# Kernel tuning notes

Hardware: AMD Instinct MI355X
Metric: run time of the kernel (lower is better)

## Reference

```python
import jax, jax.numpy as jnp
import numpy as np

FP8_MAX = 448.0  # max finite value of float8_e4m3fn


def _fp8_quant_dequant(t, scale):
    """Per-tensor static FP8 e4m3fn quantize -> dequantize (simulated real quant)."""
    q = jnp.clip(t / scale, -FP8_MAX, FP8_MAX).astype(jnp.float8_e4m3fn)
    return q.astype(jnp.float32) * scale


def setup_inputs() -> dict:
    key = jax.random.key(0)
    k1, k2, k3 = jax.random.split(key, 3)
    M, K, N = 4096, 4096, 14336  # tokens, in_features, out_features
    x = jax.random.normal(k1, (M, K), jnp.float32)
    weight = jax.random.normal(k2, (N, K), jnp.float32) * 0.02
    bias = jax.random.normal(k3, (N,), jnp.float32) * 0.01
    # static per-tensor calibration scales (amax / fp8_max)
    input_scale = (jnp.max(jnp.abs(x)) / FP8_MAX).reshape(1)
    weight_scale = (jnp.max(jnp.abs(weight)) / FP8_MAX).reshape(1)
    return {"x": x, "weight": weight, "bias": bias,
            "input_scale": input_scale, "weight_scale": weight_scale}


def reference(x, weight, bias, input_scale, weight_scale):
    # QParamsLinear forward: statically quantize input to fp8 e4m3fn with the
    # input quantizer's per-tensor scale, dequantize the fp8 weight with its
    # per-tensor scale, run the GEMM (y = x_dq @ W_dq^T), and add bias.
    s_in = input_scale[0]
    s_w = weight_scale[0]
    x_dq = _fp8_quant_dequant(x, s_in)      # [M, K]
    w_dq = _fp8_quant_dequant(weight, s_w)  # [N, K]
    return jnp.einsum('mk,nk->mn', x_dq, w_dq) + bias[None, :]
```

## Files before the change

kernel.cpp:

```cpp
#include <hip/hip_runtime.h>
#include <stdint.h>

typedef float f32x4 __attribute__((ext_vector_type(4)));

#define FP8_MAX_V 448.0f

__device__ __forceinline__ uint32_t pack4_fp8(float a, float b, float c, float d) {
    a = fminf(fmaxf(a, -FP8_MAX_V), FP8_MAX_V);
    b = fminf(fmaxf(b, -FP8_MAX_V), FP8_MAX_V);
    c = fminf(fmaxf(c, -FP8_MAX_V), FP8_MAX_V);
    d = fminf(fmaxf(d, -FP8_MAX_V), FP8_MAX_V);
    int v = 0;
    v = __builtin_amdgcn_cvt_pk_fp8_f32(a, b, v, false);
    v = __builtin_amdgcn_cvt_pk_fp8_f32(c, d, v, true);
    return (uint32_t)v;
}

__global__ void quant_fp8_kernel(const float* __restrict__ in,
                                 uint32_t* __restrict__ out,
                                 const float* __restrict__ scale_ptr,
                                 long long n4) {
    const float s = scale_ptr[0];
    long long i = (long long)blockIdx.x * blockDim.x + threadIdx.x;
    const long long stride = (long long)gridDim.x * blockDim.x;
    const float4* in4 = (const float4*)in;
    for (; i < n4; i += stride) {
        float4 v = in4[i];
        out[i] = pack4_fp8(v.x / s, v.y / s, v.z / s, v.w / s);
    }
}

__global__ __launch_bounds__(256) void gemm_fp8_kernel(
    const uint8_t* __restrict__ qA,
    const uint8_t* __restrict__ qB,
    const float* __restrict__ bias,
    const float* __restrict__ s_in_p,
    const float* __restrict__ s_w_p,
    float* __restrict__ C,
    int M, int N, int K) {
    __shared__ uint8_t lsA[128 * 128];
    __shared__ uint8_t lsB[128 * 128];

    const int tid = threadIdx.x;
    const int w   = tid >> 6;
    const int l   = tid & 63;
    const int wr  = w >> 1;
    const int wc  = w & 1;

    const int bm = blockIdx.y << 7;
    const int bn = blockIdx.x << 7;

    const float outscale = s_in_p[0] * s_w_p[0];

    f32x4 acc[4][4];
#pragma unroll
    for (int i = 0; i < 4; ++i)
#pragma unroll
        for (int j = 0; j < 4; ++j)
            acc[i][j] = (f32x4){0.f, 0.f, 0.f, 0.f};

    const int srow = l >> 3;
    const int scol = (((l & 7) ^ srow) << 4);
    const int rsw  = (l & 7) << 4;
    const int lg   = l >> 4;
    const int lr   = l & 15;

    const uint8_t* srcA0 = qA + (size_t)(bm + w * 32 + srow) * K + scol;
    const uint8_t* srcB0 = qB + (size_t)(bn + w * 32 + srow) * K + scol;

    const int nkt = K >> 7;
    for (int kt = 0; kt < nkt; ++kt) {
        const int kb = kt << 7;
#pragma unroll
        for (int i = 0; i < 4; ++i) {
            __builtin_amdgcn_global_load_lds(
                (const __attribute__((address_space(1))) void*)(srcA0 + (size_t)i * 8 * K + kb),
                (__attribute__((address_space(3))) void*)(lsA + (w * 32 + i * 8) * 128),
                16, 0, 0);
        }
#pragma unroll
        for (int i = 0; i < 4; ++i) {
            __builtin_amdgcn_global_load_lds(
                (const __attribute__((address_space(1))) void*)(srcB0 + (size_t)i * 8 * K + kb),
                (__attribute__((address_space(3))) void*)(lsB + (w * 32 + i * 8) * 128),
                16, 0, 0);
        }
        __syncthreads();

#pragma unroll
        for (int kk = 0; kk < 4; ++kk) {
            const int cswz = ((kk << 5) + (lg << 3)) ^ rsw;
            long a[4], b[4];
#pragma unroll
            for (int mi = 0; mi < 4; ++mi)
                a[mi] = *(const long*)(lsA + ((wr * 64 + mi * 16 + lr) << 7) + cswz);
#pragma unroll
            for (int ni = 0; ni < 4; ++ni)
                b[ni] = *(const long*)(lsB + ((wc * 64 + ni * 16 + lr) << 7) + cswz);
#pragma unroll
            for (int mi = 0; mi < 4; ++mi)
#pragma unroll
                for (int ni = 0; ni < 4; ++ni)
                    acc[mi][ni] = __builtin_amdgcn_mfma_f32_16x16x32_fp8_fp8(
                        a[mi], b[ni], acc[mi][ni], 0, 0, 0);
        }
        __syncthreads();
    }

    const int crow0 = bm + wr * 64 + lg * 4;
    const int ccol0 = bn + wc * 64 + lr;
#pragma unroll
    for (int ni = 0; ni < 4; ++ni) {
        const int col = ccol0 + ni * 16;
        const float bv = bias[col];
#pragma unroll
        for (int mi = 0; mi < 4; ++mi) {
            const int row = crow0 + mi * 16;
#pragma unroll
            for (int r = 0; r < 4; ++r)
                C[(size_t)(row + r) * N + col] = acc[mi][ni][r] * outscale + bv;
        }
    }
}

extern "C" void kernel_launch(void* const* d_in, const int* in_sizes, int n_in,
                              void* d_out, int out_size, void* d_ws, size_t ws_size,
                              hipStream_t stream) {
    const float* x    = (const float*)d_in[0];
    const float* wt   = (const float*)d_in[1];
    const float* bias = (const float*)d_in[2];
    const float* s_in = (const float*)d_in[3];
    const float* s_w  = (const float*)d_in[4];
    float* out = (float*)d_out;

    const long long xe = in_sizes[0];
    const long long we = in_sizes[1];
    const int N = in_sizes[2];
    const int K = (int)(we / N);
    const int M = (int)(xe / K);

    uint8_t* qx = (uint8_t*)d_ws;
    uint8_t* qw = qx + xe;

    quant_fp8_kernel<<<2048, 256, 0, stream>>>(x,  (uint32_t*)qx, s_in, xe >> 2);
    quant_fp8_kernel<<<2048, 256, 0, stream>>>(wt, (uint32_t*)qw, s_w,  we >> 2);

    dim3 grid(N / 128, M / 128);
    gemm_fp8_kernel<<<grid, 256, 0, stream>>>(qx, qw, bias, s_in, s_w, out, M, N, K);
}
```

Before: 483.9 us.

## Rewrite FP8 GEMM with 256x128 tiles, 4-stage LDS pipeline and 32x32 MFMA

```diff
diff --git a/kernel.cpp b/kernel.cpp
--- a/kernel.cpp
+++ b/kernel.cpp
@@ -1,7 +1,7 @@
 #include <hip/hip_runtime.h>
 #include <stdint.h>
 
-typedef float f32x4 __attribute__((ext_vector_type(4)));
+typedef float f32x16 __attribute__((ext_vector_type(16)));
 
 #define FP8_MAX_V 448.0f
 
@@ -30,7 +30,7 @@
     }
 }
 
-__global__ __launch_bounds__(256) void gemm_fp8_kernel(
+__global__ __launch_bounds__(512) void gemm_fp8_kernel(
     const uint8_t* __restrict__ qA,
     const uint8_t* __restrict__ qB,
     const float* __restrict__ bias,
@@ -38,89 +38,144 @@
     const float* __restrict__ s_w_p,
     float* __restrict__ C,
     int M, int N, int K) {
-    __shared__ uint8_t lsA[128 * 128];
-    __shared__ uint8_t lsB[128 * 128];
+    extern __shared__ uint8_t lds[];
 
     const int tid = threadIdx.x;
     const int w   = tid >> 6;
     const int l   = tid & 63;
     const int wr  = w >> 1;
     const int wc  = w & 1;
-
-    const int bm = blockIdx.y << 7;
-    const int bn = blockIdx.x << 7;
+    const int rl  = l & 31;
+    const int hi8 = (l >> 5) << 3;
+    const int s2  = (rl >> 1) & 3;
+
+    const int cpx = gridDim.x >> 3;
+    const int swz = ((int)blockIdx.x & 7) * cpx + ((int)blockIdx.x >> 3);
+    const int tm  = swz & 15;
+    const int tn  = swz >> 4;
+    const int bm  = tm << 8;
+    const int bn  = tn << 7;
 
     const float outscale = s_in_p[0] * s_w_p[0];
-
-    f32x4 acc[4][4];
-#pragma unroll
-    for (int i = 0; i < 4; ++i)
-#pragma unroll
-        for (int j = 0; j < 4; ++j)
-            acc[i][j] = (f32x4){0.f, 0.f, 0.f, 0.f};
-
-    const int srow = l >> 3;
-    const int scol = (((l & 7) ^ srow) << 4);
-    const int rsw  = (l & 7) << 4;
-    const int lg   = l >> 4;
-    const int lr   = l & 15;
-
-    const uint8_t* srcA0 = qA + (size_t)(bm + w * 32 + srow) * K + scol;
-    const uint8_t* srcB0 = qB + (size_t)(bn + w * 32 + srow) * K + scol;
-
-    const int nkt = K >> 7;
-    for (int kt = 0; kt < nkt; ++kt) {
-        const int kb = kt << 7;
-#pragma unroll
-        for (int i = 0; i < 4; ++i) {
-            __builtin_amdgcn_global_load_lds(
-                (const __attribute__((address_space(1))) void*)(srcA0 + (size_t)i * 8 * K + kb),
-                (__attribute__((address_space(3))) void*)(lsA + (w * 32 + i * 8) * 128),
-                16, 0, 0);
+    const int NT = K >> 6;
+
+    int colk[4];
+#pragma unroll
+    for (int kk = 0; kk < 4; ++kk) colk[kk] = ((kk ^ s2) << 4) | hi8;
+
+    const int aRowOff = (wr * 64 + rl) * 64;
+    const int bRowOff = 16384 + (wc * 64 + rl) * 64;
+
+    f32x16 acc[2][2];
+#pragma unroll
+    for (int mi = 0; mi < 2; ++mi)
+#pragma unroll
+        for (int ni = 0; ni < 2; ++ni)
+#pragma unroll
+            for (int r = 0; r < 16; ++r) acc[mi][ni][r] = 0.f;
+
+    const int strow   = tid >> 2;
+    const int stchunk = (((tid & 3) ^ ((strow >> 1) & 3)) << 4);
+    const uint8_t* srcA_t = qA + (size_t)(bm + strow) * K + stchunk;
+    const uint8_t* srcB_t = qB + (size_t)(bn + strow) * K + stchunk;
+    const int dstw = w << 10;
+
+#define STAGE_A(SLOT, KB) do { \
+    __builtin_amdgcn_global_load_lds( \
+        (const __attribute__((address_space(1))) void*)(srcA_t + (KB)), \
+        (__attribute__((address_space(3))) void*)(lds + (SLOT) * 24576 + dstw), 16, 0, 0); \
+    __builtin_amdgcn_global_load_lds( \
+        (const __attribute__((address_space(1))) void*)(srcA_t + (size_t)128 * K + (KB)), \
+        (__attribute__((address_space(3))) void*)(lds + (SLOT) * 24576 + 8192 + dstw), 16, 0, 0); \
+} while (0)
+
+#define STAGE_B(SLOT, KB) do { \
+    __builtin_amdgcn_global_load_lds( \
+        (const __attribute__((address_space(1))) void*)(srcB_t + (KB)), \
+        (__attribute__((address_space(3))) void*)(lds + (SLOT) * 24576 + 16384 + dstw), 16, 0, 0); \
+} while (0)
+
+    STAGE_A(0, 0);   STAGE_B(0, 0);
+    STAGE_A(1, 64);  STAGE_B(1, 64);
+    STAGE_A(2, 128); STAGE_B(2, 128);
+    __syncthreads();
+
+    long a[2][2], b[2][2];
+    for (int T = 0; T < NT; ++T) {
+        const int slot = T & 3;
+        const int sb   = slot * 24576;
+        const int Tp   = T + 3;
+        const int kbp  = (Tp < NT) ? (Tp << 6) : 0;
+        const int slotp = Tp & 3;
+
+        STAGE_A(slotp, kbp);
+#pragma unroll
+        for (int mi = 0; mi < 2; ++mi)
+#pragma unroll
+            for (int kk = 0; kk < 2; ++kk)
+                a[mi][kk] = *(const long*)(lds + sb + aRowOff + mi * 2048 + colk[kk]);
+#pragma unroll
+        for (int ni = 0; ni < 2; ++ni)
+#pragma unroll
+            for (int kk = 0; kk < 2; ++kk)
+                b[ni][kk] = *(const long*)(lds + sb + bRowOff + ni * 2048 + colk[kk]);
+        __builtin_amdgcn_s_barrier();
+        __builtin_amdgcn_s_setprio(1);
+#pragma unroll
+        for (int kk = 0; kk < 2; ++kk)
+#pragma unroll
+            for (int mi = 0; mi < 2; ++mi)
+#pragma unroll
+                for (int ni = 0; ni < 2; ++ni)
+                    acc[mi][ni] = __builtin_amdgcn_mfma_f32_32x32x16_fp8_fp8(
+                        a[mi][kk], b[ni][kk], acc[mi][ni], 0, 0, 0);
+        __builtin_amdgcn_s_setprio(0);
+        __builtin_amdgcn_s_barrier();
+
+        STAGE_B(slotp, kbp);
+#pragma unroll
+        for (int mi = 0; mi < 2; ++mi)
+#pragma unroll
+            for (int kk = 0; kk < 2; ++kk)
+                a[mi][kk] = *(const long*)(lds + sb + aRowOff + mi * 2048 + colk[kk + 2]);
+#pragma unroll
+        for (int ni = 0; ni < 2; ++ni)
+#pragma unroll
+            for (int kk = 0; kk < 2; ++kk)
+                b[ni][kk] = *(const long*)(lds + sb + bRowOff + ni * 2048 + colk[kk + 2]);
+        __builtin_amdgcn_s_barrier();
+        __builtin_amdgcn_s_setprio(1);
+#pragma unroll
+        for (int kk = 0; kk < 2; ++kk)
+#pragma unroll
+            for (int mi = 0; mi < 2; ++mi)
+#pragma unroll
+                for (int ni = 0; ni < 2; ++ni)
+                    acc[mi][ni] = __builtin_amdgcn_mfma_f32_32x32x16_fp8_fp8(
+                        a[mi][kk], b[ni][kk], acc[mi][ni], 0, 0, 0);
+        __builtin_amdgcn_s_setprio(0);
+        asm volatile("s_waitcnt vmcnt(6)" ::: "memory");
+        __builtin_amdgcn_s_barrier();
+    }
+
+    const int crow0 = bm + wr * 64 + ((l >> 5) << 2);
+    const int ccol0 = bn + wc * 64 + rl;
+    const float bv0 = bias[ccol0];
+    const float bv1 = bias[ccol0 + 32];
+#pragma unroll
+    for (int mi = 0; mi < 2; ++mi)
+#pragma unroll
+        for (int ni = 0; ni < 2; ++ni) {
+            const float bv = ni ? bv1 : bv0;
+            const int col = ccol0 + ni * 32;
+#pragma unroll
+            for (int r = 0; r < 16; ++r) {
+                const int row = crow0 + mi * 32 + (r & 3) + ((r >> 2) << 3);
+                C[(size_t)row * N + col] = acc[mi][ni][r] * outscale + bv;
+            }
         }
-#pragma unroll
-        for (int i = 0; i < 4; ++i) {
-            __builtin_amdgcn_global_load_lds(
-                (const __attribute__((address_space(1))) void*)(srcB0 + (size_t)i * 8 * K + kb),
-                (__attribute__((address_space(3))) void*)(lsB + (w * 32 + i * 8) * 128),
-                16, 0, 0);
-        }
-        __syncthreads();
-
-#pragma unroll
-        for (int kk = 0; kk < 4; ++kk) {
-            const int cswz = ((kk << 5) + (lg << 3)) ^ rsw;
-            long a[4], b[4];
-#pragma unroll
-            for (int mi = 0; mi < 4; ++mi)
-                a[mi] = *(const long*)(lsA + ((wr * 64 + mi * 16 + lr) << 7) + cswz);
-#pragma unroll
-            for (int ni = 0; ni < 4; ++ni)
-                b[ni] = *(const long*)(lsB + ((wc * 64 + ni * 16 + lr) << 7) + cswz);
-#pragma unroll
-            for (int mi = 0; mi < 4; ++mi)
-#pragma unroll
-                for (int ni = 0; ni < 4; ++ni)
-                    acc[mi][ni] = __builtin_amdgcn_mfma_f32_16x16x32_fp8_fp8(
-                        a[mi], b[ni], acc[mi][ni], 0, 0, 0);
-        }
-        __syncthreads();
-    }
-
-    const int crow0 = bm + wr * 64 + lg * 4;
-    const int ccol0 = bn + wc * 64 + lr;
-#pragma unroll
-    for (int ni = 0; ni < 4; ++ni) {
-        const int col = ccol0 + ni * 16;
-        const float bv = bias[col];
-#pragma unroll
-        for (int mi = 0; mi < 4; ++mi) {
-            const int row = crow0 + mi * 16;
-#pragma unroll
-            for (int r = 0; r < 4; ++r)
-                C[(size_t)(row + r) * N + col] = acc[mi][ni][r] * outscale + bv;
-        }
-    }
+#undef STAGE_A
+#undef STAGE_B
 }
 
 extern "C" void kernel_launch(void* const* d_in, const int* in_sizes, int n_in,
@@ -145,6 +200,7 @@
     quant_fp8_kernel<<<2048, 256, 0, stream>>>(x,  (uint32_t*)qx, s_in, xe >> 2);
     quant_fp8_kernel<<<2048, 256, 0, stream>>>(wt, (uint32_t*)qw, s_w,  we >> 2);
 
-    dim3 grid(N / 128, M / 128);
-    gemm_fp8_kernel<<<grid, 256, 0, stream>>>(qx, qw, bias, s_in, s_w, out, M, N, K);
-}
+    dim3 grid((N / 128) * (M / 256));
+    gemm_fp8_kernel<<<grid, 512, 98304, stream>>>(qx, qw, bias, s_in, s_w, out,
+                                                  M, N, K);
+}
```

New measurement: 529.3 us. +9.4%, slower.

## Rewrite FP8 GEMM with 256x128 tiles, 4-stage LDS pipeline and XCD block swizzle

Applied to the files above, without the earlier changes.

```diff
diff --git a/kernel.cpp b/kernel.cpp
--- a/kernel.cpp
+++ b/kernel.cpp
@@ -30,7 +30,7 @@
     }
 }
 
-__global__ __launch_bounds__(256) void gemm_fp8_kernel(
+__global__ __launch_bounds__(512, 2) void gemm_fp8_kernel(
     const uint8_t* __restrict__ qA,
     const uint8_t* __restrict__ qB,
     const float* __restrict__ bias,
@@ -38,76 +38,125 @@
     const float* __restrict__ s_w_p,
     float* __restrict__ C,
     int M, int N, int K) {
-    __shared__ uint8_t lsA[128 * 128];
-    __shared__ uint8_t lsB[128 * 128];
+    extern __shared__ uint8_t lds[];
 
     const int tid = threadIdx.x;
     const int w   = tid >> 6;
     const int l   = tid & 63;
     const int wr  = w >> 1;
     const int wc  = w & 1;
-
-    const int bm = blockIdx.y << 7;
-    const int bn = blockIdx.x << 7;
+    const int lr  = l & 15;
+    const int lg  = l >> 4;
+    const int fl  = (lr >> 1) & 3;
+    const int h8  = (lg & 1) << 3;
+    const int cg0 = lg >> 1;
+
+    const int cpx = (int)gridDim.x >> 3;
+    const int swz = ((int)blockIdx.x & 7) * cpx + ((int)blockIdx.x >> 3);
+    const int bm  = (swz & 15) << 8;
+    const int bn  = (swz >> 4) << 7;
 
     const float outscale = s_in_p[0] * s_w_p[0];
+    const int NT = K >> 6;
+
+    int aOff[2], bOff[2];
+#pragma unroll
+    for (int k = 0; k < 2; ++k) {
+        const int chunk = ((k * 2 + cg0) ^ fl) << 4;
+        aOff[k] = (wr * 64 + lr) * 64 + chunk + h8;
+        bOff[k] = 16384 + (wc * 64 + lr) * 64 + chunk + h8;
+    }
 
     f32x4 acc[4][4];
 #pragma unroll
-    for (int i = 0; i < 4; ++i)
-#pragma unroll
-        for (int j = 0; j < 4; ++j)
-            acc[i][j] = (f32x4){0.f, 0.f, 0.f, 0.f};
-
-    const int srow = l >> 3;
-    const int scol = (((l & 7) ^ srow) << 4);
-    const int rsw  = (l & 7) << 4;
-    const int lg   = l >> 4;
-    const int lr   = l & 15;
-
-    const uint8_t* srcA0 = qA + (size_t)(bm + w * 32 + srow) * K + scol;
-    const uint8_t* srcB0 = qB + (size_t)(bn + w * 32 + srow) * K + scol;
-
-    const int nkt = K >> 7;
-    for (int kt = 0; kt < nkt; ++kt) {
-        const int kb = kt << 7;
-#pragma unroll
-        for (int i = 0; i < 4; ++i) {
-            __builtin_amdgcn_global_load_lds(
-                (const __attribute__((address_space(1))) void*)(srcA0 + (size_t)i * 8 * K + kb),
-                (__attribute__((address_space(3))) void*)(lsA + (w * 32 + i * 8) * 128),
-                16, 0, 0);
-        }
-#pragma unroll
-        for (int i = 0; i < 4; ++i) {
-            __builtin_amdgcn_global_load_lds(
-                (const __attribute__((address_space(1))) void*)(srcB0 + (size_t)i * 8 * K + kb),
-                (__attribute__((address_space(3))) void*)(lsB + (w * 32 + i * 8) * 128),
-                16, 0, 0);
-        }
-        __syncthreads();
-
-#pragma unroll
-        for (int kk = 0; kk < 4; ++kk) {
-            const int cswz = ((kk << 5) + (lg << 3)) ^ rsw;
-            long a[4], b[4];
+    for (int mi = 0; mi < 4; ++mi)
+#pragma unroll
+        for (int ni = 0; ni < 4; ++ni)
+            acc[mi][ni] = (f32x4){0.f, 0.f, 0.f, 0.f};
+
+    const int strow  = tid >> 2;
+    const int schunk = (((tid & 3) ^ ((strow >> 1) & 3)) << 4);
+    const uint8_t* sA = qA + (size_t)(bm + strow) * K + schunk;
+    const uint8_t* sB = qB + (size_t)(bn + strow) * K + schunk;
+    const int dstw = w << 10;
+
+#define STAGE_A(SL, KB) do { \
+    __builtin_amdgcn_global_load_lds( \
+        (const __attribute__((address_space(1))) void*)(sA + (KB)), \
+        (__attribute__((address_space(3))) void*)(lds + (SL) * 24576 + dstw), 16, 0, 0); \
+    __builtin_amdgcn_global_load_lds( \
+        (const __attribute__((address_space(1))) void*)(sA + (size_t)128 * K + (KB)), \
+        (__attribute__((address_space(3))) void*)(lds + (SL) * 24576 + 8192 + dstw), 16, 0, 0); \
+} while (0)
+#define STAGE_B(SL, KB) do { \
+    __builtin_amdgcn_global_load_lds( \
+        (const __attribute__((address_space(1))) void*)(sB + (KB)), \
+        (__attribute__((address_space(3))) void*)(lds + (SL) * 24576 + 16384 + dstw), 16, 0, 0); \
+} while (0)
+
+    STAGE_A(0, 0);   STAGE_B(0, 0);
+    STAGE_A(1, 64);  STAGE_B(1, 64);
+    STAGE_A(2, 128); STAGE_B(2, 128);
+    asm volatile("s_waitcnt vmcnt(6)" ::: "memory");
+    __builtin_amdgcn_s_barrier();
+
+    long a[4][2], b[2][2];
+    for (int T = 0; T < NT; ++T) {
+        const uint8_t* sbase = lds + (T & 3) * 24576;
+        const int Tp  = T + 3;
+        const int kbp = (Tp < NT ? Tp : 0) << 6;
+        const int slp = Tp & 3;
+
+        STAGE_A(slp, kbp);
+#pragma unroll
+        for (int mi = 0; mi < 4; ++mi)
+#pragma unroll
+            for (int k = 0; k < 2; ++k)
+                a[mi][k] = *(const long*)(sbase + aOff[k] + mi * 1024);
+#pragma unroll
+        for (int ni = 0; ni < 2; ++ni)
+#pragma unroll
+            for (int k = 0; k < 2; ++k)
+                b[ni][k] = *(const long*)(sbase + bOff[k] + ni * 1024);
+        __builtin_amdgcn_s_barrier();
+        asm volatile("s_waitcnt lgkmcnt(0)" ::: "memory");
+        __builtin_amdgcn_sched_barrier(0);
+        __builtin_amdgcn_s_setprio(1);
+#pragma unroll
+        for (int k = 0; k < 2; ++k)
 #pragma unroll
             for (int mi = 0; mi < 4; ++mi)
-                a[mi] = *(const long*)(lsA + ((wr * 64 + mi * 16 + lr) << 7) + cswz);
-#pragma unroll
-            for (int ni = 0; ni < 4; ++ni)
-                b[ni] = *(const long*)(lsB + ((wc * 64 + ni * 16 + lr) << 7) + cswz);
+#pragma unroll
+                for (int ni = 0; ni < 2; ++ni)
+                    acc[mi][ni] = __builtin_amdgcn_mfma_f32_16x16x32_fp8_fp8(
+                        a[mi][k], b[ni][k], acc[mi][ni], 0, 0, 0);
+        __builtin_amdgcn_s_setprio(0);
+        __builtin_amdgcn_s_barrier();
+
+        STAGE_B(slp, kbp);
+#pragma unroll
+        for (int ni = 0; ni < 2; ++ni)
+#pragma unroll
+            for (int k = 0; k < 2; ++k)
+                b[ni][k] = *(const long*)(sbase + bOff[k] + (ni + 2) * 1024);
+        __builtin_amdgcn_s_barrier();
+        asm volatile("s_waitcnt lgkmcnt(0)" ::: "memory");
+        __builtin_amdgcn_sched_barrier(0);
+        __builtin_amdgcn_s_setprio(1);
+#pragma unroll
+        for (int k = 0; k < 2; ++k)
 #pragma unroll
             for (int mi = 0; mi < 4; ++mi)
 #pragma unroll
-                for (int ni = 0; ni < 4; ++ni)
-                    acc[mi][ni] = __builtin_amdgcn_mfma_f32_16x16x32_fp8_fp8(
-                        a[mi], b[ni], acc[mi][ni], 0, 0, 0);
-        }
-        __syncthreads();
-    }
-
-    const int crow0 = bm + wr * 64 + lg * 4;
+                for (int ni = 0; ni < 2; ++ni)
+                    acc[mi][ni + 2] = __builtin_amdgcn_mfma_f32_16x16x32_fp8_fp8(
+                        a[mi][k], b[ni][k], acc[mi][ni + 2], 0, 0, 0);
+        __builtin_amdgcn_s_setprio(0);
+        asm volatile("s_waitcnt vmcnt(6)" ::: "memory");
+        __builtin_amdgcn_s_barrier();
+    }
+
+    const int crow0 = bm + wr * 64 + (lg << 2);
     const int ccol0 = bn + wc * 64 + lr;
 #pragma unroll
     for (int ni = 0; ni < 4; ++ni) {
@@ -121,6 +170,8 @@
                 C[(size_t)(row + r) * N + col] = acc[mi][ni][r] * outscale + bv;
         }
     }
+#undef STAGE_A
+#undef STAGE_B
 }
 
 extern "C" void kernel_launch(void* const* d_in, const int* in_sizes, int n_in,
@@ -145,6 +196,7 @@
     quant_fp8_kernel<<<2048, 256, 0, stream>>>(x,  (uint32_t*)qx, s_in, xe >> 2);
     quant_fp8_kernel<<<2048, 256, 0, stream>>>(wt, (uint32_t*)qw, s_w,  we >> 2);
 
-    dim3 grid(N / 128, M / 128);
-    gemm_fp8_kernel<<<grid, 256, 0, stream>>>(qx, qw, bias, s_in, s_w, out, M, N, K);
-}
+    dim3 grid((N / 128) * (M / 256));
+    gemm_fp8_kernel<<<grid, 512, 98304, stream>>>(qx, qw, bias, s_in, s_w, out,
+                                                  M, N, K);
+}
```

New measurement: 543.8 us. +12.4%, slower.

## Use MX-scaled 16x16x128 FP8 MFMA with XCD-aware block swizzle

Applied to the files above, without the earlier changes.

```diff
diff --git a/kernel.cpp b/kernel.cpp
--- a/kernel.cpp
+++ b/kernel.cpp
@@ -2,6 +2,8 @@
 #include <stdint.h>
 
 typedef float f32x4 __attribute__((ext_vector_type(4)));
+typedef int   i32x8 __attribute__((ext_vector_type(8)));
+typedef long  i64x2 __attribute__((ext_vector_type(2)));
 
 #define FP8_MAX_V 448.0f
 
@@ -30,7 +32,7 @@
     }
 }
 
-__global__ __launch_bounds__(256) void gemm_fp8_kernel(
+__global__ __launch_bounds__(256, 3) void gemm_mxfp8_kernel(
     const uint8_t* __restrict__ qA,
     const uint8_t* __restrict__ qB,
     const float* __restrict__ bias,
@@ -46,68 +48,82 @@
     const int l   = tid & 63;
     const int wr  = w >> 1;
     const int wc  = w & 1;
+    const int lr  = l & 15;
+    const int lg  = l >> 4;
+    const int lsw = lr & 7;
 
-    const int bm = blockIdx.y << 7;
-    const int bn = blockIdx.x << 7;
+    const int cpx = (int)gridDim.x >> 3;
+    const int swz = ((int)blockIdx.x & 7) * cpx + ((int)blockIdx.x >> 3);
+    const int bm  = (swz & 31) << 7;
+    const int bn  = (swz >> 5) << 7;
 
     const float outscale = s_in_p[0] * s_w_p[0];
+    const int NT = K >> 7;
+
+    const int off0 = (((lg << 1) ^ lsw) << 4);
+    const int off1 = off0 ^ 16;
 
     f32x4 acc[4][4];
 #pragma unroll
-    for (int i = 0; i < 4; ++i)
+    for (int mi = 0; mi < 4; ++mi)
 #pragma unroll
-        for (int j = 0; j < 4; ++j)
-            acc[i][j] = (f32x4){0.f, 0.f, 0.f, 0.f};
+        for (int ni = 0; ni < 4; ++ni)
+            acc[mi][ni] = (f32x4){0.f, 0.f, 0.f, 0.f};
 
-    const int srow = l >> 3;
-    const int scol = (((l & 7) ^ srow) << 4);
-    const int rsw  = (l & 7) << 4;
-    const int lg   = l >> 4;
-    const int lr   = l & 15;
+    const int srow = tid >> 3;
+    const int sc   = (((tid & 7) ^ (srow & 7)) << 4);
+    const uint8_t* sA = qA + (size_t)(bm + srow) * K + sc;
+    const uint8_t* sB = qB + (size_t)(bn + srow) * K + sc;
+    const int dstw = w << 10;
 
-    const uint8_t* srcA0 = qA + (size_t)(bm + w * 32 + srow) * K + scol;
-    const uint8_t* srcB0 = qB + (size_t)(bn + w * 32 + srow) * K + scol;
+    union frag { i32x8 v; i64x2 h[2]; };
 
-    const int nkt = K >> 7;
-    for (int kt = 0; kt < nkt; ++kt) {
+    for (int kt = 0; kt < NT; ++kt) {
         const int kb = kt << 7;
 #pragma unroll
         for (int i = 0; i < 4; ++i) {
             __builtin_amdgcn_global_load_lds(
-                (const __attribute__((address_space(1))) void*)(srcA0 + (size_t)i * 8 * K + kb),
-                (__attribute__((address_space(3))) void*)(lsA + (w * 32 + i * 8) * 128),
-                16, 0, 0);
+                (const __attribute__((address_space(1))) void*)(sA + (size_t)(i * 32) * K + kb),
+                (__attribute__((address_space(3))) void*)(lsA + i * 4096 + dstw), 16, 0, 0);
         }
 #pragma unroll
         for (int i = 0; i < 4; ++i) {
             __builtin_amdgcn_global_load_lds(
-                (const __attribute__((address_space(1))) void*)(srcB0 + (size_t)i * 8 * K + kb),
-                (__attribute__((address_space(3))) void*)(lsB + (w * 32 + i * 8) * 128),
-                16, 0, 0);
+                (const __attribute__((address_space(1))) void*)(sB + (size_t)(i * 32) * K + kb),
+                (__attribute__((address_space(3))) void*)(lsB + i * 4096 + dstw), 16, 0, 0);
         }
         __syncthreads();
 
+        i32x8 a[4], b[4];
 #pragma unroll
-        for (int kk = 0; kk < 4; ++kk) {
-            const int cswz = ((kk << 5) + (lg << 3)) ^ rsw;
-            long a[4], b[4];
+        for (int mi = 0; mi < 4; ++mi) {
+            const uint8_t* base = lsA + ((wr * 64 + mi * 16 + lr) << 7);
+            frag u;
+            u.h[0] = *(const i64x2*)(base + off0);
+            u.h[1] = *(const i64x2*)(base + off1);
+            a[mi] = u.v;
+        }
 #pragma unroll
-            for (int mi = 0; mi < 4; ++mi)
-                a[mi] = *(const long*)(lsA + ((wr * 64 + mi * 16 + lr) << 7) + cswz);
+        for (int ni = 0; ni < 4; ++ni) {
+            const uint8_t* base = lsB + ((wc * 64 + ni * 16 + lr) << 7);
+            frag u;
+            u.h[0] = *(const i64x2*)(base + off0);
+            u.h[1] = *(const i64x2*)(base + off1);
+            b[ni] = u.v;
+        }
+#pragma unroll
+        for (int mi = 0; mi < 4; ++mi)
 #pragma unroll
             for (int ni = 0; ni < 4; ++ni)
-                b[ni] = *(const long*)(lsB + ((wc * 64 + ni * 16 + lr) << 7) + cswz);
-#pragma unroll
-            for (int mi = 0; mi < 4; ++mi)
-#pragma unroll
-                for (int ni = 0; ni < 4; ++ni)
-                    acc[mi][ni] = __builtin_amdgcn_mfma_f32_16x16x32_fp8_fp8(
-                        a[mi], b[ni], acc[mi][ni], 0, 0, 0);
-        }
+                acc[mi][ni] = __builtin_amdgcn_mfma_scale_f32_16x16x128_f8f6f4(
+                    a[mi], b[ni], acc[mi][ni],
+                    0, 0,
+                    0, 127,
+                    0, 127);
         __syncthreads();
     }
 
-    const int crow0 = bm + wr * 64 + lg * 4;
+    const int crow0 = bm + wr * 64 + (lg << 2);
     const int ccol0 = bn + wc * 64 + lr;
 #pragma unroll
     for (int ni = 0; ni < 4; ++ni) {
@@ -145,6 +161,7 @@
     quant_fp8_kernel<<<2048, 256, 0, stream>>>(x,  (uint32_t*)qx, s_in, xe >> 2);
     quant_fp8_kernel<<<2048, 256, 0, stream>>>(wt, (uint32_t*)qw, s_w,  we >> 2);
 
-    dim3 grid(N / 128, M / 128);
-    gemm_fp8_kernel<<<grid, 256, 0, stream>>>(qx, qw, bias, s_in, s_w, out, M, N, K);
+    dim3 grid((M / 128) * (N / 128));
+    gemm_mxfp8_kernel<<<grid, 256, 0, stream>>>(qx, qw, bias, s_in, s_w, out,
+                                                M, N, K);
 }
```

Result: faster. 396.5 us (-18.1%).
